# Performance work log

Hardware: AMD Instinct MI355X
Metric: run time of the kernel (lower is better)

## Reference

```python
import jax, jax.numpy as jnp
import numpy as np

N = 512      # nodes
F_IN = 16    # raw node features; adjacency channels = 2*F_IN = 32
H = 64       # hidden
HF = 64      # hidden_final
C = 10       # num_classes
L = 3        # num_layers
E = 16384    # edges (avg degree 32)
EPS = 1e-5


def setup_inputs() -> dict:
    key = jax.random.key(0)
    ks = iter(jax.random.split(key, 40))
    rn = lambda shape, s=0.05: jax.random.normal(next(ks), shape, jnp.float32) * s
    inp = {
        'x': jax.random.normal(next(ks), (N, F_IN), jnp.float32),
        'edge_index': jax.random.randint(next(ks), (2, E), 0, N),
        # no_prop FeatureExtractor
        'np1_w': rn((HF, 2 * F_IN)), 'np1_b': rn((HF,)),
        'np2_w': rn((HF, 2 * F_IN)), 'np3_w': rn((HF, HF)),
        # first PowerfulLayer (in = 2*F_IN)
        'c0_m1_w': rn((H, 2 * F_IN)), 'c0_m1_b': rn((H,)),
        'c0_m2_w': rn((H, 2 * F_IN)), 'c0_m2_b': rn((H,)),
        'c0_m4_w': rn((H, 2 * F_IN + H)), 'c0_m4_b': rn((H,)),
        # remaining L-1 PowerfulLayers (stacked)
        'cm1_w': rn((L - 1, H, H)), 'cm1_b': rn((L - 1, H)),
        'cm2_w': rn((L - 1, H, H)), 'cm2_b': rn((L - 1, H)),
        'cm4_w': rn((L - 1, H, 2 * H)), 'cm4_b': rn((L - 1, H)),
        # batchnorms (training-mode stats; affine params)
        'bn_g': jnp.ones((L, H), jnp.float32), 'bn_b': jnp.zeros((L, H), jnp.float32),
        # per-layer FeatureExtractors (stacked)
        'fe1_w': rn((L, HF, H)), 'fe1_b': rn((L, HF)),
        'fe2_w': rn((L, HF, H)), 'fe3_w': rn((L, HF, HF)),
        # after_conv and final linear
        'ac_w': rn((HF, HF)), 'ac_b': rn((HF,)),
        'fl_w': rn((C, HF)), 'fl_b': rn((C,)),
    }
    return inp


def _lin(x, w, b=None):
    y = x @ w.T
    return y if b is None else y + b


def _extractor(u, w1, b1, w2, w3):
    # u: [B, N, N, F]; graph_class=True, aggr='add'
    n = u.shape[1]
    trace = jnp.einsum('biif->bf', u)                     # sum of diagonal entries
    out1 = _lin(trace / n, w1, b1)
    s = (u.sum(axis=(1, 2)) - trace) / (n * (n - 1))      # off-diagonal mean-ish
    out = out1 + _lin(s, w2)
    return out + _lin(jax.nn.relu(out), w3)


def _powerful(u, m1w, m1b, m2w, m2b, m4w, m4b):
    # UnitMLP with 1 layer == 1x1 conv == per-position linear (no ReLU)
    o1 = jnp.einsum('bijc,oc->bijo', u, m1w) + m1b        # [B,N,N,H]
    o2 = jnp.einsum('bijc,oc->bijo', u, m2w) + m2b
    mult = jnp.einsum('bikh,bkjh->bijh', o1, o2)          # per-channel NxN matmul
    return _lin(jnp.concatenate([mult, u], axis=-1), m4w, m4b)


def _batchnorm(u, g, b):
    # BatchNorm2d in training mode: stats over (batch, N, N) per channel, biased var
    mean = u.mean(axis=(0, 1, 2))
    var = u.var(axis=(0, 1, 2))
    return (u - mean) * jax.lax.rsqrt(var + EPS) * g + b


def reference(x, edge_index, np1_w, np1_b, np2_w, np3_w,
              c0_m1_w, c0_m1_b, c0_m2_w, c0_m2_b, c0_m4_w, c0_m4_b,
              cm1_w, cm1_b, cm2_w, cm2_b, cm4_w, cm4_b,
              bn_g, bn_b, fe1_w, fe1_b, fe2_w, fe3_w,
              ac_w, ac_b, fl_w, fl_b):
    n = x.shape[0]
    src, dst = edge_index[0], edge_index[1]
    edge_attr = jnp.concatenate([x[src], x[dst]], axis=-1)          # [E, 2F]
    A = jnp.zeros((n, n, edge_attr.shape[-1]), x.dtype).at[src, dst].add(edge_attr)
    u = A[None]                                                      # [1,N,N,2F]

    out = _extractor(u, np1_w, np1_b, np2_w, np3_w)
    nlayers = bn_g.shape[0]
    for l in range(nlayers):
        if l == 0:
            u = _powerful(u, c0_m1_w, c0_m1_b, c0_m2_w, c0_m2_b, c0_m4_w, c0_m4_b)
        else:
            u = _powerful(u, cm1_w[l - 1], cm1_b[l - 1], cm2_w[l - 1], cm2_b[l - 1],
                          cm4_w[l - 1], cm4_b[l - 1])
        u = _batchnorm(u, bn_g[l], bn_b[l])
        out = out + _extractor(u, fe1_w[l], fe1_b[l], fe2_w[l], fe3_w[l])

    out = jax.nn.relu(out) / nlayers
    out = out + jax.nn.relu(_lin(out, ac_w, ac_b))   # layer_after_conv
    # dropout with p=0.0 / eval mode is identity
    out = _lin(out, fl_w, fl_b)
    return jax.nn.log_softmax(out, axis=-1)          # [1, num_classes]
```

## Files before the change

kernel.cpp:

```cpp
#include <hip/hip_runtime.h>
#include <hip/hip_bf16.h>

#define Nn   512
#define NN   262144
#define EDG  16384

typedef unsigned short u16;
typedef unsigned int u32;
typedef short v8s __attribute__((ext_vector_type(8)));
typedef float v4f __attribute__((ext_vector_type(4)));
typedef u16 u16x8 __attribute__((ext_vector_type(8)));

__device__ __forceinline__ float b2f(u16 u) {
    union { unsigned int i; float f; } v; v.i = ((unsigned int)u) << 16; return v.f;
}
__device__ __forceinline__ u16 f2b(float f) {
    union { float f; unsigned int i; } v; v.f = f;
    unsigned int r = (v.i + 0x7FFFu + ((v.i >> 16) & 1u)) >> 16;
    return (u16)r;
}
__device__ __forceinline__ u32 aff2(u32 x, float s, float h) {
    float lo = b2f((u16)(x & 0xFFFFu)) * s + h;
    float hi = b2f((u16)(x >> 16)) * s + h;
    return (u32)f2b(lo) | ((u32)f2b(hi) << 16);
}

__global__ void sentinel_kernel(float* __restrict__ out, float val) {
    if (threadIdx.x < 10) out[threadIdx.x] = val;
}

__global__ void cvt_weights(const float* __restrict__ s0, const float* __restrict__ s1,
                            const float* __restrict__ s2, const float* __restrict__ s3,
                            const float* __restrict__ s4, const float* __restrict__ s5,
                            u16* __restrict__ dst) {
    int t = blockIdx.x * 256 + threadIdx.x;
    if (t >= 43008) return;
    float v;
    if      (t < 2048)  v = s0[t];
    else if (t < 4096)  v = s1[t - 2048];
    else if (t < 10240) v = s2[t - 4096];
    else if (t < 18432) v = s3[t - 10240];
    else if (t < 26624) v = s4[t - 18432];
    else                v = s5[t - 26624];
    dst[t] = f2b(v);
}

__global__ void scatter_edges(const float* __restrict__ x, const int* __restrict__ ei,
                              float* __restrict__ A) {
    int t = blockIdx.x * 256 + threadIdx.x;
    if (t >= EDG * 32) return;
    int e = t >> 5, c = t & 31;
    int s = ei[e], d = ei[EDG + e];
    float v = (c < 16) ? x[s * 16 + c] : x[d * 16 + (c - 16)];
    atomicAdd(A + ((size_t)s * Nn + d) * 32 + c, v);
}

__global__ __launch_bounds__(256) void finalize_u0(const float* __restrict__ A,
                                                   u16* __restrict__ u0,
                                                   float* __restrict__ total) {
    __shared__ u16 L[32 * 258];
    __shared__ float red[4][32];
    int t = threadIdx.x;
    int p0 = blockIdx.x * 256;
    const float* Ar = A + (size_t)(p0 + t) * 32;
    float v[32];
#pragma unroll
    for (int c = 0; c < 32; ++c) v[c] = Ar[c];
#pragma unroll
    for (int c = 0; c < 32; ++c) L[c * 258 + t] = f2b(v[c]);
    int wv = t >> 6;
#pragma unroll
    for (int c = 0; c < 32; ++c) {
        float r = v[c];
        for (int off = 32; off > 0; off >>= 1) r += __shfl_down(r, off);
        if ((t & 63) == 0) red[wv][c] = r;
    }
    __syncthreads();
    if (t < 32) atomicAdd(total + t, red[0][t] + red[1][t] + red[2][t] + red[3][t]);
    int off = (t & 31) * 8, rb = t >> 5;
#pragma unroll
    for (int pass = 0; pass < 4; ++pass) {
        int c = pass * 8 + rb;
        u16x8 w = *(const u16x8*)(L + c * 258 + off);
        *(u16x8*)(u0 + (size_t)c * NN + p0 + off) = w;
    }
}

__global__ void trace_raw_cm(const u16* __restrict__ ucm, float* __restrict__ trraw) {
    int c = blockIdx.x, t = threadIdx.x;
    const u16* base = ucm + (size_t)c * NN;
    float s = b2f(base[(size_t)(2 * t) * 513]) + b2f(base[(size_t)(2 * t + 1) * 513]);
    for (int off = 32; off > 0; off >>= 1) s += __shfl_down(s, off);
    __shared__ float r[4];
    if ((t & 63) == 0) r[t >> 6] = s;
    __syncthreads();
    if (t == 0) trraw[c] = r[0] + r[1] + r[2] + r[3];
}

template<int CIN>
__global__ __launch_bounds__(512, 4) void conv12_s(
    const u16* __restrict__ src,
    const float* __restrict__ sc, const float* __restrict__ sh,
    const u16* __restrict__ w1, const float* __restrict__ b1,
    const u16* __restrict__ w2, const float* __restrict__ b2,
    u16* __restrict__ dst1, u16* __restrict__ dst2)
{
    constexpr int G    = CIN / 8;
    constexpr int LOGG = (CIN == 64) ? 3 : 2;
    constexpr int ROWB = CIN * 2;
    constexpr int KC   = CIN / 32;
    constexpr int PASSES = CIN / 32;

    __shared__ char LB[2][128 * ROWB];

    const int t = threadIdx.x;
    const int lane = t & 63, w = t >> 6;
    const int l15 = lane & 15, quad = lane >> 4;
    const int wr = w >> 1;
    const int wn = w & 1;
    const size_t Pblk = (size_t)blockIdx.x * 512;

    const int cpair = (CIN == 64) ? (t >> 4) : (t >> 5);
    const int pg    = (CIN == 64) ? (t & 15) : (t & 31);
    const int g0    = cpair >> 2;
    const int word  = cpair & 3;
    const u16* srcA = src + (size_t)(2 * cpair) * NN;
    float s0 = 1.f, h0 = 0.f, s1 = 1.f, h1 = 0.f;
    const bool aff = (sc != nullptr);
    if (aff) { s0 = sc[2 * cpair]; h0 = sh[2 * cpair]; s1 = sc[2 * cpair + 1]; h1 = sh[2 * cpair + 1]; }

    v8s af[2][KC];
#pragma unroll
    for (int mt = 0; mt < 2; ++mt) {
        const int row = wr * 32 + mt * 16 + l15;
        const u16* Wm = (row < 64) ? (w1 + row * CIN) : (w2 + (row - 64) * CIN);
#pragma unroll
        for (int kc = 0; kc < KC; ++kc)
            af[mt][kc] = *(const v8s*)(Wm + kc * 32 + quad * 8);
    }
    float bias[2][4];
#pragma unroll
    for (int mt = 0; mt < 2; ++mt)
#pragma unroll
        for (int r = 0; r < 4; ++r) {
            const int row = wr * 32 + mt * 16 + quad * 4 + r;
            bias[mt][r] = (row < 64) ? b1[row] : b2[row - 64];
        }

    v4f acc[2][4];
#pragma unroll
    for (int mt = 0; mt < 2; ++mt)
#pragma unroll
        for (int nt = 0; nt < 4; ++nt) acc[mt][nt] = (v4f){0.f, 0.f, 0.f, 0.f};

    uint2 ea[PASSES], eb[PASSES];

#define C12_LOAD(T)                                                           \
    _Pragma("unroll")                                                         \
    for (int pp = 0; pp < PASSES; ++pp) {                                     \
        const int p0_ = (pg + ((CIN == 64) ? 16 : 0) * pp) * 4;               \
        const u16* sp_ = srcA + Pblk + (size_t)(T) * 128 + p0_;               \
        ea[pp] = *(const uint2*)sp_;                                          \
        eb[pp] = *(const uint2*)(sp_ + NN);                                   \
    }

#define C12_WRITE(BUF)                                                        \
    {                                                                         \
        char* Lb_ = LB[BUF];                                                  \
        _Pragma("unroll")                                                     \
        for (int pp = 0; pp < PASSES; ++pp) {                                 \
            const int p0_ = (pg + ((CIN == 64) ? 16 : 0) * pp) * 4;           \
            u32 A0 = ea[pp].x, A1 = ea[pp].y, B0 = eb[pp].x, B1 = eb[pp].y;   \
            if (aff) {                                                        \
                A0 = aff2(A0, s0, h0); A1 = aff2(A1, s0, h0);                 \
                B0 = aff2(B0, s1, h1); B1 = aff2(B1, s1, h1);                 \
            }                                                                 \
            u32 pk0 = (A0 & 0xFFFFu) | (B0 << 16);                            \
            u32 pk1 = (A0 >> 16) | (B0 & 0xFFFF0000u);                        \
            u32 pk2 = (A1 & 0xFFFFu) | (B1 << 16);                            \
            u32 pk3 = (A1 >> 16) | (B1 & 0xFFFF0000u);                        \
            _Pragma("unroll")                                                 \
            for (int w4 = 0; w4 < 4; ++w4) {                                  \
                const int p_ = p0_ + w4;                                      \
                const int g_ = g0 ^ (p_ & (G - 1)) ^ ((p_ >> LOGG) & (G - 1));\
                u32 v_ = (w4 == 0) ? pk0 : (w4 == 1) ? pk1 : (w4 == 2) ? pk2 : pk3; \
                *(u32*)(Lb_ + p_ * ROWB + g_ * 16 + word * 4) = v_;           \
            }                                                                 \
        }                                                                     \
    }

#define C12_COMPUTE(BUF)                                                      \
    _Pragma("unroll")                                                         \
    for (int kc = 0; kc < KC; ++kc) {                                         \
        v8s bf_[4];                                                           \
        const char* Lb_ = LB[BUF];                                            \
        _Pragma("unroll")                                                     \
        for (int nt = 0; nt < 4; ++nt) {                                      \
            const int p_ = wn * 64 + nt * 16 + l15;                           \
            const int lg_ = kc * 4 + quad;                                    \
            const int g_ = lg_ ^ (p_ & (G - 1)) ^ ((p_ >> LOGG) & (G - 1));   \
            bf_[nt] = *(const v8s*)(Lb_ + p_ * ROWB + g_ * 16);               \
        }                                                                     \
        _Pragma("unroll")                                                     \
        for (int mt = 0; mt < 2; ++mt)                                        \
            _Pragma("unroll")                                                 \
            for (int nt = 0; nt < 4; ++nt)                                    \
                acc[mt][nt] = __builtin_amdgcn_mfma_f32_16x16x32_bf16(        \
                    af[mt][kc], bf_[nt], acc[mt][nt], 0, 0, 0);               \
    }

    C12_LOAD(0)
    C12_WRITE(0)
    __syncthreads();

#pragma unroll
    for (int T = 0; T < 4; ++T) {
        const int cur = T & 1;
        if (T < 3) C12_LOAD(T + 1)
        C12_COMPUTE(cur)
#pragma unroll
        for (int mt = 0; mt < 2; ++mt)
#pragma unroll
            for (int r = 0; r < 4; ++r) {
                const int row = wr * 32 + mt * 16 + quad * 4 + r;
                u16* dp = ((row < 64) ? (dst1 + (size_t)row * NN)
                                      : (dst2 + (size_t)(row - 64) * NN))
                          + Pblk + (size_t)T * 128 + wn * 64 + l15;
#pragma unroll
                for (int nt = 0; nt < 4; ++nt) {
                    u16 v = f2b(acc[mt][nt][r] + bias[mt][r]);
                    __builtin_nontemporal_store(v, dp + nt * 16);
                }
            }
#pragma unroll
        for (int mt = 0; mt < 2; ++mt)
#pragma unroll
            for (int nt = 0; nt < 4; ++nt) acc[mt][nt] = (v4f){0.f,0.f,0.f,0.f};
        if (T < 3) {
            C12_WRITE(cur ^ 1)
            __syncthreads();
        }
    }
#undef C12_LOAD
#undef C12_WRITE
#undef C12_COMPUTE
}

template<int NCH>
__global__ __launch_bounds__(256) void conv4_t(
    const u16* __restrict__ mult, const u16* __restrict__ u,
    const float* __restrict__ sc, const float* __restrict__ sh,
    const u16* __restrict__ w, const float* __restrict__ bias,
    u16* __restrict__ dst,
    float* __restrict__ psum, float* __restrict__ psq, float* __restrict__ ptr)
{
    __shared__ u16 LS[8320];
    __shared__ float R1[64][4], R2[64][4];
    const int K = NCH * 32;
    const int t = threadIdx.x;
    const int P0 = blockIdx.x * 128;
    const int lane = t & 63, wave = t >> 6;
    const int l15 = lane & 15, quad = lane >> 4;
    const int pw = wave * 32;
    const int sr = t >> 4;
    const int so = (t & 15) * 8;

    u16x8 pf[NCH][2];
#pragma unroll
    for (int kc = 0; kc < NCH; ++kc)
#pragma unroll
        for (int ps = 0; ps < 2; ++ps) {
            int cg = kc * 32 + ps * 16 + sr;
            const u16* gp = (cg < 64) ? (mult + (size_t)cg * NN + P0 + so)
                                      : (u + (size_t)(cg - 64) * NN + P0 + so);
            pf[kc][ps] = *(const u16x8*)gp;
        }

    v4f acc[4][2];
#pragma unroll
    for (int mt = 0; mt < 4; ++mt)
#pragma unroll
        for (int nt = 0; nt < 2; ++nt) acc[mt][nt] = (v4f){0.f, 0.f, 0.f, 0.f};

#pragma unroll
    for (int ps = 0; ps < 2; ++ps)
        *(u16x8*)(LS + (ps * 16 + sr) * 130 + so) = pf[0][ps];
    __syncthreads();
#pragma unroll
    for (int kc = 0; kc < NCH; ++kc) {
        if (kc + 1 < NCH) {
            u16* Ln = LS + ((kc + 1) & 1) * 4160;
#pragma unroll
            for (int ps = 0; ps < 2; ++ps) {
                int c = ps * 16 + sr;
                int cg = (kc + 1) * 32 + c;
                u16x8 v = pf[kc + 1][ps];
                if (cg >= 64 && sc) {
                    float s = sc[cg - 64], f = sh[cg - 64];
#pragma unroll
                    for (int j = 0; j < 8; ++j) v[j] = f2b(b2f(v[j]) * s + f);
                }
                *(u16x8*)(Ln + c * 130 + so) = v;
            }
        }
        v8s af[4];
#pragma unroll
        for (int mt = 0; mt < 4; ++mt)
            af[mt] = *(const v8s*)(w + (mt * 16 + l15) * K + kc * 32 + quad * 8);
        const u16* Lb = LS + (kc & 1) * 4160;
#pragma unroll
        for (int nt = 0; nt < 2; ++nt) {
            const int p = pw + nt * 16 + l15;
            v8s b;
#pragma unroll
            for (int j = 0; j < 8; ++j) b[j] = (short)Lb[(quad * 8 + j) * 130 + p];
#pragma unroll
            for (int mt = 0; mt < 4; ++mt)
                acc[mt][nt] = __builtin_amdgcn_mfma_f32_16x16x32_bf16(af[mt], b, acc[mt][nt], 0, 0, 0);
        }
        if (kc + 1 < NCH) __syncthreads();
    }
    __syncthreads();
#pragma unroll
    for (int mt = 0; mt < 4; ++mt)
#pragma unroll
        for (int r = 0; r < 4; ++r) {
            const int h = mt * 16 + quad * 4 + r;
            const float bv = bias[h];
#pragma unroll
            for (int nt = 0; nt < 2; ++nt)
                LS[h * 130 + pw + nt * 16 + l15] = f2b(acc[mt][nt][r] + bv);
        }
    __syncthreads();
    {
        int c = t >> 2, q = t & 3;
        const u16* row = LS + c * 130 + q * 32;
        float s = 0.f, s2 = 0.f;
#pragma unroll
        for (int i = 0; i < 32; ++i) { float v = b2f(row[i]); s += v; s2 += v * v; }
        R1[c][q] = s; R2[c][q] = s2;
    }
    __syncthreads();
    {
        int i = P0 >> 9, j0 = P0 & 511;
        int blk = blockIdx.x;
        if (t < 64) {
            psum[t * 2048 + blk] = R1[t][0] + R1[t][1] + R1[t][2] + R1[t][3];
            psq[t * 2048 + blk]  = R2[t][0] + R2[t][1] + R2[t][2] + R2[t][3];
            if (j0 <= i && i < j0 + 128) ptr[t * 512 + i] = b2f(LS[t * 130 + (i - j0)]);
        }
    }
#pragma unroll
    for (int ps = 0; ps < 4; ++ps) {
        int h = ps * 16 + sr;
        u16x8 v = *(const u16x8*)(LS + h * 130 + so);
        __builtin_nontemporal_store(v, (u16x8*)(dst + (size_t)h * NN + P0 + so));
    }
}

__global__ __launch_bounds__(512, 2) void bmm_mfma256(const u16* __restrict__ Aall,
                                                      const u16* __restrict__ Ball,
                                                      u16* __restrict__ Call) {
    __shared__ u16 LA[2][16384];
    __shared__ u16 LB[2][16384];

    const int bid = blockIdx.x;
    const int h  = ((bid >> 5) << 3) | (bid & 7);
    const int qq = (bid >> 3) & 3;
    const int ty = qq >> 1, tx = qq & 1;
    const int t = threadIdx.x;
    const int l = t & 63, w = t >> 6;
    const int l15 = l & 15, quad = l >> 4;
    const int wr = w >> 2, wc = w & 3;

    const u16* Ap = Aall + (size_t)h * NN + (size_t)ty * 256 * 512;
    const u16* Bp = Ball + (size_t)h * NN + tx * 256;
    u16* Cp = Call + (size_t)h * NN;

    const int a_m = l >> 3;
    const int a_kg = (l & 7) ^ a_m;
    const u16* ApL = Ap + (size_t)a_m * 512 + a_kg * 8;

    v4f acc[8][4];
#pragma unroll
    for (int mt = 0; mt < 8; ++mt)
#pragma unroll
        for (int nt = 0; nt < 4; ++nt) acc[mt][nt] = (v4f){0.f, 0.f, 0.f, 0.f};

    uint2 eB[4], oB[4];

#define BMM_BLOAD(K0)                                                         \
    _Pragma("unroll")                                                         \
    for (int L = 0; L < 4; ++L) {                                             \
        const int p = w + 8 * L;                                              \
        const u16* s_ = Bp + (size_t)((K0) + 2 * p) * 512 + l * 4;            \
        eB[L] = *(const uint2*)s_;                                            \
        oB[L] = *(const uint2*)(s_ + 512);                                    \
    }

#define BMM_ALOAD(BUF, K0)                                                    \
    _Pragma("unroll")                                                         \
    for (int c = 0; c < 4; ++c) {                                             \
        const int cc = w * 4 + c;                                             \
        __builtin_amdgcn_global_load_lds(                                     \
            (const void*)(ApL + (size_t)cc * 4096 + (K0)),                    \
            (void*)&LA[BUF][cc * 512], 16, 0, 0);                             \
    }

#define BMM_BWRITE(BUF)                                                       \
    {                                                                         \
        char* base_ = (char*)&LB[BUF][0];                                     \
        _Pragma("unroll")                                                     \
        for (int L = 0; L < 4; ++L) {                                         \
            const int p = w + 8 * L;                                          \
            const int gk = p >> 2, wd = p & 3;                                \
            u32 e0 = eB[L].x, e1 = eB[L].y, o0 = oB[L].x, o1 = oB[L].y;       \
            u32 pk0 = (e0 & 0xFFFFu) | (o0 << 16);                            \
            u32 pk1 = (e0 >> 16) | (o0 & 0xFFFF0000u);                        \
            u32 pk2 = (e1 & 0xFFFFu) | (o1 << 16);                            \
            u32 pk3 = (e1 >> 16) | (o1 & 0xFFFF0000u);                        \
            _Pragma("unroll")                                                 \
            for (int q = 0; q < 4; ++q) {                                     \
                const int j = l * 4 + q;                                      \
                const int g = gk ^ (j & 7) ^ ((j >> 3) & 7);                  \
                u32 v_ = (q == 0) ? pk0 : (q == 1) ? pk1 : (q == 2) ? pk2 : pk3; \
                *(u32*)(base_ + j * 128 + (g << 4) + wd * 4) = v_;            \
            }                                                                 \
        }                                                                     \
    }

#define BMM_COMPUTE(BUF)                                                      \
    _Pragma("unroll")                                                         \
    for (int kk = 0; kk < 2; ++kk) {                                          \
        v8s af_[8], bf_[4];                                                   \
        const char* baseA_ = (const char*)&LA[BUF][0];                        \
        const char* baseB_ = (const char*)&LB[BUF][0];                        \
        _Pragma("unroll")                                                     \
        for (int mt = 0; mt < 8; ++mt) {                                      \
            const int m = wr * 128 + mt * 16 + l15;                           \
            const int g = (kk * 4 + quad) ^ (m & 7);                          \
            af_[mt] = *(const v8s*)(baseA_ + m * 128 + (g << 4));             \
        }                                                                     \
        _Pragma("unroll")                                                     \
        for (int nt = 0; nt < 4; ++nt) {                                      \
            const int j = wc * 64 + nt * 16 + l15;                            \
            const int g = (kk * 4 + quad) ^ (j & 7) ^ ((j >> 3) & 7);         \
            bf_[nt] = *(const v8s*)(baseB_ + j * 128 + (g << 4));             \
        }                                                                     \
        _Pragma("unroll")                                                     \
        for (int mt = 0; mt < 8; ++mt)                                        \
            _Pragma("unroll")                                                 \
            for (int nt = 0; nt < 4; ++nt)                                    \
                acc[mt][nt] = __builtin_amdgcn_mfma_f32_16x16x32_bf16(        \
                    af_[mt], bf_[nt], acc[mt][nt], 0, 0, 0);                  \
    }

    BMM_BLOAD(0)
    BMM_ALOAD(0, 0)
    BMM_BWRITE(0)
    __syncthreads();

#pragma unroll 2
    for (int ts = 0; ts < 8; ++ts) {
        const int cur = ts & 1;
        if (ts < 7) {
            BMM_BLOAD((ts + 1) * 64)
            BMM_ALOAD(cur ^ 1, (ts + 1) * 64)
        }
        BMM_COMPUTE(cur)
        if (ts < 7) {
            BMM_BWRITE(cur ^ 1)
            __syncthreads();
        }
    }

#pragma unroll
    for (int mt = 0; mt < 8; ++mt)
#pragma unroll
        for (int r = 0; r < 4; ++r) {
            const int i = ty * 256 + wr * 128 + mt * 16 + quad * 4 + r;
#pragma unroll
            for (int nt = 0; nt < 4; ++nt) {
                const int j = tx * 256 + wc * 64 + nt * 16 + l15;
                Cp[(size_t)i * 512 + j] = f2b(acc[mt][nt][r]);
            }
        }
#undef BMM_BLOAD
#undef BMM_ALOAD
#undef BMM_BWRITE
#undef BMM_COMPUTE
}

__global__ __launch_bounds__(256) void bn_finalize(
    const float* __restrict__ psum, const float* __restrict__ psq,
    const float* __restrict__ ptr,
    const float* __restrict__ g, const float* __restrict__ b,
    float* __restrict__ scale, float* __restrict__ shift,
    float* __restrict__ ttl) {
    int c = blockIdx.x, t = threadIdx.x;
    float s = 0.f, q = 0.f, tr = 0.f;
    for (int k = t; k < 2048; k += 256) { s += psum[c * 2048 + k]; q += psq[c * 2048 + k]; }
    for (int k = t; k < 512; k += 256) tr += ptr[c * 512 + k];
    for (int off = 32; off > 0; off >>= 1) {
        s += __shfl_down(s, off); q += __shfl_down(q, off); tr += __shfl_down(tr, off);
    }
    __shared__ float r1[4], r2[4], r3[4];
    if ((t & 63) == 0) { r1[t >> 6] = s; r2[t >> 6] = q; r3[t >> 6] = tr; }
    __syncthreads();
    if (t == 0) {
        s = r1[0] + r1[1] + r1[2] + r1[3];
        q = r2[0] + r2[1] + r2[2] + r2[3];
        tr = r3[0] + r3[1] + r3[2] + r3[3];
        float mean = s * (1.f / 262144.f);
        float var = q * (1.f / 262144.f) - mean * mean;
        float sc = g[c] * rsqrtf(fmaxf(var, 0.f) + 1e-5f);
        float sh = b[c] - mean * sc;
        scale[c] = sc;
        shift[c] = sh;
        ttl[64 + c] = sc * s + 262144.f * sh;
        ttl[c]      = sc * tr + 512.f * sh;
    }
}

__global__ __launch_bounds__(256) void extractor_par(
    const float* __restrict__ tt,
    const float* __restrict__ np1w, const float* __restrict__ np1b,
    const float* __restrict__ np2w, const float* __restrict__ np3w,
    const float* __restrict__ fe1w, const float* __restrict__ fe1b,
    const float* __restrict__ fe2w, const float* __restrict__ fe3w,
    float* __restrict__ oacc_part) {
    __shared__ float red[64][4];
    __shared__ float xo[64];
    const int li = blockIdx.x;
    const int t = threadIdx.x;
    const int h = t >> 2, q = t & 3;
    const int C = (li == 0) ? 32 : 64;
    const float* w1 = (li == 0) ? np1w : fe1w + (li - 1) * 4096;
    const float* b1 = (li == 0) ? np1b : fe1b + (li - 1) * 64;
    const float* w2 = (li == 0) ? np2w : fe2w + (li - 1) * 4096;
    const float* w3 = (li == 0) ? np3w : fe3w + (li - 1) * 4096;
    const float* tr = tt + li * 128;
    const float* to = tr + 64;
    const int cpq = C >> 2;
    float p = 0.f;
    for (int i = 0; i < cpq; ++i) {
        int c = q * cpq + i;
        p += (tr[c] * (1.f / 512.f)) * w1[h * C + c]
           + ((to[c] - tr[c]) * (1.f / (512.f * 511.f))) * w2[h * C + c];
    }
    red[h][q] = p;
    __syncthreads();
    if (q == 0) xo[h] = b1[h] + red[h][0] + red[h][1] + red[h][2] + red[h][3];
    __syncthreads();
    float o = xo[h];
    float p3 = 0.f;
    for (int i = 0; i < 16; ++i) {
        int f = q * 16 + i;
        p3 += fmaxf(xo[f], 0.f) * w3[h * 64 + f];
    }
    __syncthreads();
    red[h][q] = p3;
    __syncthreads();
    if (q == 0) oacc_part[li * 64 + h] = o + red[h][0] + red[h][1] + red[h][2] + red[h][3];
}

__global__ __launch_bounds__(256) void head_par(
    const float* __restrict__ oacc_part,
    const float* __restrict__ acw, const float* __restrict__ acb,
    const float* __restrict__ flw, const float* __restrict__ flb,
    float* __restrict__ out) {
    __shared__ float x[64], x2[64], red[64][4], l[10];
    const int t = threadIdx.x;
    const int h = t >> 2, q = t & 3;
    if (q == 0) {
        float oa = oacc_part[h] + oacc_part[64 + h] + oacc_part[128 + h] + oacc_part[192 + h];
        x[h] = fmaxf(oa, 0.f) * (1.f / 3.f);
    }
    __syncthreads();
    float p = 0.f;
    for (int i = 0; i < 16; ++i) { int f = q * 16 + i; p += x[f] * acw[h * 64 + f]; }
    red[h][q] = p;
    __syncthreads();
    if (q == 0) {
        float y = acb[h] + red[h][0] + red[h][1] + red[h][2] + red[h][3];
        x2[h] = x[h] + fmaxf(y, 0.f);
    }
    __syncthreads();
    if (t < 40) {
        int hh = t >> 2, qq = t & 3;
        float p2 = 0.f;
        for (int i = 0; i < 16; ++i) { int f = qq * 16 + i; p2 += x2[f] * flw[hh * 64 + f]; }
        red[hh][qq] = p2;
    }
    __syncthreads();
    if (t < 10) l[t] = flb[t] + red[t][0] + red[t][1] + red[t][2] + red[t][3];
    __syncthreads();
    if (t == 0) {
        float m = l[0];
        for (int i = 1; i < 10; ++i) m = fmaxf(m, l[i]);
        float se = 0.f;
        for (int i = 0; i < 10; ++i) se += expf(l[i] - m);
        float ls = m + logf(se);
        for (int i = 0; i < 10; ++i) out[i] = l[i] - ls;
    }
}

extern "C" void kernel_launch(void* const* d_in, const int* in_sizes, int n_in,
                              void* d_out, int out_size, void* d_ws, size_t ws_size,
                              hipStream_t stream) {
    float* out = (float*)d_out;

    static const int exp_sizes[28] = {
        8192, 32768,
        2048, 64, 2048, 4096,
        2048, 64, 2048, 64, 6144, 64,
        8192, 128, 8192, 128, 16384, 128,
        192, 192,
        12288, 192, 12288, 12288,
        4096, 64, 640, 10
    };
    bool ok = (n_in == 28);
    if (ok) for (int i = 0; i < 28; ++i) if (in_sizes[i] != exp_sizes[i]) ok = false;
    if (!ok) { sentinel_kernel<<<1, 64, 0, stream>>>(out, -5.0f); return; }

    const size_t RSZ = (size_t)NN * 64 * 2;
    const size_t BIG_OFF = 8192 + 90112;
    if (ws_size < BIG_OFF + 4 * RSZ) {
        sentinel_kernel<<<1, 64, 0, stream>>>(out, -7.0f);
        return;
    }

    const float* x     = (const float*)d_in[0];
    const int*   ei    = (const int*)d_in[1];
    const float* np1w  = (const float*)d_in[2];
    const float* np1b  = (const float*)d_in[3];
    const float* np2w  = (const float*)d_in[4];
    const float* np3w  = (const float*)d_in[5];
    const float* c0m1b = (const float*)d_in[7];
    const float* c0m2b = (const float*)d_in[9];
    const float* c0m4b = (const float*)d_in[11];
    const float* cm1b  = (const float*)d_in[13];
    const float* cm2b  = (const float*)d_in[15];
    const float* cm4b  = (const float*)d_in[17];
    const float* bng   = (const float*)d_in[18];
    const float* bnb   = (const float*)d_in[19];
    const float* fe1w  = (const float*)d_in[20];
    const float* fe1b  = (const float*)d_in[21];
    const float* fe2w  = (const float*)d_in[22];
    const float* fe3w  = (const float*)d_in[23];
    const float* acw   = (const float*)d_in[24];
    const float* acb   = (const float*)d_in[25];
    const float* flw   = (const float*)d_in[26];
    const float* flb   = (const float*)d_in[27];

    char* ws = (char*)d_ws;
    float* small = (float*)ws;
    float* tt    = small;
    float* scl   = small + 512;
    float* shf   = small + 576;
    float* oaccp = small + 640;

    u16* arena = (u16*)(ws + 8192);

    char* big = ws + BIG_OFF;
    u16* S0 = (u16*)(big + 0 * RSZ);
    u16* S1 = (u16*)(big + 1 * RSZ);
    u16* S2 = (u16*)(big + 2 * RSZ);
    u16* S3 = (u16*)(big + 3 * RSZ);
    float* Abuf = (float*)S2;

    float* psum = (float*)S2;
    float* psq  = psum + 64 * 2048;
    float* ptr  = psq + 64 * 2048;

    hipMemsetAsync(small, 0, 4096, stream);
    hipMemsetAsync(Abuf, 0, (size_t)NN * 32 * 4, stream);

    cvt_weights<<<168, 256, 0, stream>>>((const float*)d_in[6], (const float*)d_in[8],
                                         (const float*)d_in[10], (const float*)d_in[12],
                                         (const float*)d_in[14], (const float*)d_in[16], arena);
    scatter_edges<<<2048, 256, 0, stream>>>(x, ei, Abuf);
    finalize_u0<<<1024, 256, 0, stream>>>(Abuf, S0, tt + 64);
    trace_raw_cm<<<32, 256, 0, stream>>>(S0, tt);

    u16* U[3]  = { S0, S1, S0 };
    u16* O1[3] = { S1, S0, S1 };
    u16* R[3]  = { S1, S0, S1 };

    const float *aff_s = nullptr, *aff_h = nullptr;

    for (int l = 0; l < 3; ++l) {
        int Cin = (l == 0) ? 32 : 64;
        const u16 *w1b, *w2b, *w4b;
        const float *b1, *b2, *b4;
        if (l == 0) {
            w1b = arena;            b1 = c0m1b;
            w2b = arena + 2048;     b2 = c0m2b;
            w4b = arena + 4096;     b4 = c0m4b;
        } else {
            int m = l - 1;
            w1b = arena + 10240 + m * 4096;  b1 = cm1b + m * 64;
            w2b = arena + 18432 + m * 4096;  b2 = cm2b + m * 64;
            w4b = arena + 26624 + m * 8192;  b4 = cm4b + m * 64;
        }
        if (Cin == 32)
            conv12_s<32><<<512, 512, 0, stream>>>(U[l], aff_s, aff_h, w1b, b1, w2b, b2, O1[l], S2);
        else
            conv12_s<64><<<512, 512, 0, stream>>>(U[l], aff_s, aff_h, w1b, b1, w2b, b2, O1[l], S2);
        bmm_mfma256<<<256, 512, 0, stream>>>(O1[l], S2, S3);
        if (Cin == 32)
            conv4_t<3><<<2048, 256, 0, stream>>>(S3, U[l], aff_s, aff_h, w4b, b4, R[l], psum, psq, ptr);
        else
            conv4_t<4><<<2048, 256, 0, stream>>>(S3, U[l], aff_s, aff_h, w4b, b4, R[l], psum, psq, ptr);
        bn_finalize<<<64, 256, 0, stream>>>(psum, psq, ptr, bng + l * 64, bnb + l * 64,
                                            scl, shf, tt + (l + 1) * 128);
        aff_s = scl; aff_h = shf;
    }
    extractor_par<<<4, 256, 0, stream>>>(tt, np1w, np1b, np2w, np3w,
                                         fe1w, fe1b, fe2w, fe3w, oaccp);
    head_par<<<1, 256, 0, stream>>>(oaccp, acw, acb, flw, flb, out);
}
```

Measured before the change: 462.3 us.

## Add double-buffered streaming conv4 kernel for 64-channel layers

Replaces the conv4_t<4> launch (2048 blocks of 256 threads) for the 64-channel layers with a new conv4_s kernel, launched as 512 blocks of 512 threads. Each block processes one row of 512 positions in four 128-position steps. Weights stay in registers, and input tiles are double-buffered through swizzled LDS so global loads for the next step overlap the MFMA work on the current one. BatchNorm partial sums are reduced per block, and bn_finalize now takes the block count as a parameter. The intent is to amortise weight loads and cut block count and partial-sum traffic, at the cost of more LDS and register pressure per block.

```diff
diff --git a/kernel.cpp b/kernel.cpp
--- a/kernel.cpp
+++ b/kernel.cpp
@@ -246,6 +246,179 @@
 #undef C12_COMPUTE
 }
 
+__global__ __launch_bounds__(512, 4) void conv4_s(
+    const u16* __restrict__ mult, const u16* __restrict__ u,
+    const float* __restrict__ sc, const float* __restrict__ sh,
+    const u16* __restrict__ w, const float* __restrict__ bias,
+    u16* __restrict__ dst,
+    float* __restrict__ psum, float* __restrict__ psq, float* __restrict__ ptr)
+{
+    constexpr int ROWB = 256;
+    __shared__ char LB[2][128 * ROWB];
+    __shared__ float R1[64][4], R2[64][4];
+
+    const int t = threadIdx.x;
+    const int lane = t & 63, w8 = t >> 6;
+    const int l15 = lane & 15, quad = lane >> 4;
+    const int wr = w8 >> 2;
+    const int wn = w8 & 3;
+    const int brow = blockIdx.x;
+    const size_t Pblk = (size_t)brow * 512;
+
+    const int pair = t >> 3;
+    const int pg = t & 7;
+    const int g0 = pair >> 2;
+    const int word = pair & 3;
+    const bool isU = pair >= 32;
+    const u16* srcA = isU ? (u + (size_t)(2 * pair - 64) * NN)
+                          : (mult + (size_t)(2 * pair) * NN);
+    float s0 = 1.f, h0 = 0.f, s1 = 1.f, h1 = 0.f;
+    const bool doaff = isU && (sc != nullptr);
+    if (doaff) { s0 = sc[2 * pair - 64]; h0 = sh[2 * pair - 64];
+                 s1 = sc[2 * pair - 63]; h1 = sh[2 * pair - 63]; }
+
+    v8s af[2][4];
+#pragma unroll
+    for (int mt = 0; mt < 2; ++mt) {
+        const int row = wr * 32 + mt * 16 + l15;
+#pragma unroll
+        for (int kc = 0; kc < 4; ++kc)
+            af[mt][kc] = *(const v8s*)(w + row * 128 + kc * 32 + quad * 8);
+    }
+    float bv_[2][4];
+#pragma unroll
+    for (int mt = 0; mt < 2; ++mt)
+#pragma unroll
+        for (int r = 0; r < 4; ++r)
+            bv_[mt][r] = bias[wr * 32 + mt * 16 + quad * 4 + r];
+
+    v4f acc[2][2];
+    float bnS[2][4], bnQ[2][4];
+#pragma unroll
+    for (int mt = 0; mt < 2; ++mt) {
+#pragma unroll
+        for (int nt = 0; nt < 2; ++nt) acc[mt][nt] = (v4f){0.f, 0.f, 0.f, 0.f};
+#pragma unroll
+        for (int r = 0; r < 4; ++r) { bnS[mt][r] = 0.f; bnQ[mt][r] = 0.f; }
+    }
+
+    uint2 ea[4], eb[4];
+
+#define C4_LOAD(T)                                                            \
+    _Pragma("unroll")                                                         \
+    for (int pp = 0; pp < 4; ++pp) {                                          \
+        const int p0_ = (pg + 8 * pp) * 4;                                    \
+        const u16* sp_ = srcA + Pblk + (size_t)(T) * 128 + p0_;               \
+        ea[pp] = *(const uint2*)sp_;                                          \
+        eb[pp] = *(const uint2*)(sp_ + NN);                                   \
+    }
+
+#define C4_WRITE(BUF)                                                         \
+    {                                                                         \
+        char* Lb_ = LB[BUF];                                                  \
+        _Pragma("unroll")                                                     \
+        for (int pp = 0; pp < 4; ++pp) {                                      \
+            const int p0_ = (pg + 8 * pp) * 4;                                \
+            u32 A0 = ea[pp].x, A1 = ea[pp].y, B0 = eb[pp].x, B1 = eb[pp].y;   \
+            if (doaff) {                                                      \
+                A0 = aff2(A0, s0, h0); A1 = aff2(A1, s0, h0);                 \
+                B0 = aff2(B0, s1, h1); B1 = aff2(B1, s1, h1);                 \
+            }                                                                 \
+            u32 pk0 = (A0 & 0xFFFFu) | (B0 << 16);                            \
+            u32 pk1 = (A0 >> 16) | (B0 & 0xFFFF0000u);                        \
+            u32 pk2 = (A1 & 0xFFFFu) | (B1 << 16);                            \
+            u32 pk3 = (A1 >> 16) | (B1 & 0xFFFF0000u);                        \
+            _Pragma("unroll")                                                 \
+            for (int w4 = 0; w4 < 4; ++w4) {                                  \
+                const int p_ = p0_ + w4;                                      \
+                const int g_ = g0 ^ (p_ & 15) ^ ((p_ >> 4) & 15);             \
+                u32 v_ = (w4 == 0) ? pk0 : (w4 == 1) ? pk1 : (w4 == 2) ? pk2 : pk3; \
+                *(u32*)(Lb_ + p_ * ROWB + g_ * 16 + word * 4) = v_;           \
+            }                                                                 \
+        }                                                                     \
+    }
+
+#define C4_COMPUTE(BUF)                                                       \
+    _Pragma("unroll")                                                         \
+    for (int kc = 0; kc < 4; ++kc) {                                          \
+        v8s bf_[2];                                                           \
+        const char* Lb_ = LB[BUF];                                            \
+        _Pragma("unroll")                                                     \
+        for (int nt = 0; nt < 2; ++nt) {                                      \
+            const int p_ = wn * 32 + nt * 16 + l15;                           \
+            const int lg_ = kc * 4 + quad;                                    \
+            const int g_ = lg_ ^ (p_ & 15) ^ ((p_ >> 4) & 15);                \
+            bf_[nt] = *(const v8s*)(Lb_ + p_ * ROWB + g_ * 16);               \
+        }                                                                     \
+        _Pragma("unroll")                                                     \
+        for (int mt = 0; mt < 2; ++mt)                                        \
+            _Pragma("unroll")                                                 \
+            for (int nt = 0; nt < 2; ++nt)                                    \
+                acc[mt][nt] = __builtin_amdgcn_mfma_f32_16x16x32_bf16(        \
+                    af[mt][kc], bf_[nt], acc[mt][nt], 0, 0, 0);               \
+    }
+
+    C4_LOAD(0)
+    C4_WRITE(0)
+    __syncthreads();
+
+#pragma unroll
+    for (int T = 0; T < 4; ++T) {
+        const int cur = T & 1;
+        if (T < 3) C4_LOAD(T + 1)
+        C4_COMPUTE(cur)
+#pragma unroll
+        for (int mt = 0; mt < 2; ++mt)
+#pragma unroll
+            for (int r = 0; r < 4; ++r) {
+                const int c = wr * 32 + mt * 16 + quad * 4 + r;
+#pragma unroll
+                for (int nt = 0; nt < 2; ++nt) {
+                    const int pos = T * 128 + wn * 32 + nt * 16 + l15;
+                    float fv = acc[mt][nt][r] + bv_[mt][r];
+                    u16 b16 = f2b(fv);
+                    float rv = b2f(b16);
+                    bnS[mt][r] += rv;
+                    bnQ[mt][r] += rv * rv;
+                    __builtin_nontemporal_store(b16, dst + (size_t)c * NN + Pblk + pos);
+                    if (pos == brow) ptr[c * 512 + brow] = rv;
+                }
+            }
+#pragma unroll
+        for (int mt = 0; mt < 2; ++mt)
+#pragma unroll
+            for (int nt = 0; nt < 2; ++nt) acc[mt][nt] = (v4f){0.f, 0.f, 0.f, 0.f};
+        if (T < 3) {
+            C4_WRITE(cur ^ 1)
+            __syncthreads();
+        }
+    }
+
+#pragma unroll
+    for (int mt = 0; mt < 2; ++mt)
+#pragma unroll
+        for (int r = 0; r < 4; ++r) {
+            float s = bnS[mt][r], q = bnQ[mt][r];
+#pragma unroll
+            for (int m = 1; m < 16; m <<= 1) {
+                s += __shfl_xor(s, m);
+                q += __shfl_xor(q, m);
+            }
+            if (l15 == 0) {
+                const int c = wr * 32 + mt * 16 + quad * 4 + r;
+                R1[c][wn] = s; R2[c][wn] = q;
+            }
+        }
+    __syncthreads();
+    if (t < 64) {
+        psum[t * 2048 + brow] = R1[t][0] + R1[t][1] + R1[t][2] + R1[t][3];
+        psq[t * 2048 + brow]  = R2[t][0] + R2[t][1] + R2[t][2] + R2[t][3];
+    }
+#undef C4_LOAD
+#undef C4_WRITE
+#undef C4_COMPUTE
+}
+
 template<int NCH>
 __global__ __launch_bounds__(256) void conv4_t(
     const u16* __restrict__ mult, const u16* __restrict__ u,
@@ -496,10 +669,10 @@
     const float* __restrict__ ptr,
     const float* __restrict__ g, const float* __restrict__ b,
     float* __restrict__ scale, float* __restrict__ shift,
-    float* __restrict__ ttl) {
+    float* __restrict__ ttl, int nblk) {
     int c = blockIdx.x, t = threadIdx.x;
     float s = 0.f, q = 0.f, tr = 0.f;
-    for (int k = t; k < 2048; k += 256) { s += psum[c * 2048 + k]; q += psq[c * 2048 + k]; }
+    for (int k = t; k < nblk; k += 256) { s += psum[c * 2048 + k]; q += psq[c * 2048 + k]; }
     for (int k = t; k < 512; k += 256) tr += ptr[c * 512 + k];
     for (int off = 32; off > 0; off >>= 1) {
         s += __shfl_down(s, off); q += __shfl_down(q, off); tr += __shfl_down(tr, off);
@@ -708,12 +881,16 @@
         else
             conv12_s<64><<<512, 512, 0, stream>>>(U[l], aff_s, aff_h, w1b, b1, w2b, b2, O1[l], S2);
         bmm_mfma256<<<256, 512, 0, stream>>>(O1[l], S2, S3);
-        if (Cin == 32)
+        int nblk;
+        if (Cin == 32) {
             conv4_t<3><<<2048, 256, 0, stream>>>(S3, U[l], aff_s, aff_h, w4b, b4, R[l], psum, psq, ptr);
-        else
-            conv4_t<4><<<2048, 256, 0, stream>>>(S3, U[l], aff_s, aff_h, w4b, b4, R[l], psum, psq, ptr);
+            nblk = 2048;
+        } else {
+            conv4_s<<<512, 512, 0, stream>>>(S3, U[l], aff_s, aff_h, w4b, b4, R[l], psum, psq, ptr);
+            nblk = 512;
+        }
         bn_finalize<<<64, 256, 0, stream>>>(psum, psq, ptr, bng + l * 64, bnb + l * 64,
-                                            scl, shf, tt + (l + 1) * 128);
+                                            scl, shf, tt + (l + 1) * 128, nblk);
         aff_s = scl; aff_h = shf;
     }
     extractor_par<<<4, 256, 0, stream>>>(tt, np1w, np1b, np2w, np3w,
```

Result: slower. 498.5 us (+7.8%).
